# Kernel optimization log

Hardware: AMD Instinct MI355X
Metric: run time of the kernel (lower is better)

## Reference

```python
import jax, jax.numpy as jnp
import numpy as np


def _lstm_last(x, w_ih, w_hh, b_ih, b_hh):
    # x: [M, T, D] -> last hidden state [M, H]; PyTorch gate order i,f,g,o
    M = x.shape[0]
    H = w_hh.shape[1]
    xi = jnp.einsum('mtd,gd->tmg', x, w_ih) + b_ih + b_hh  # [T, M, 4H]
    def step(carry, xt):
        h, c = carry
        gates = xt + h @ w_hh.T
        i, f, g, o = jnp.split(gates, 4, axis=-1)
        c = jax.nn.sigmoid(f) * c + jax.nn.sigmoid(i) * jnp.tanh(g)
        h = jax.nn.sigmoid(o) * jnp.tanh(c)
        return (h, c), None
    z = jnp.zeros((M, H), x.dtype)
    (h, _), _ = jax.lax.scan(step, (z, z), xi)
    return h


def _gcn_conv(x, edge_index, w, b):
    # Symmetric-normalized GCN conv with self loops (PyG GCNConv defaults).
    # x: [BT, N, F] -> [BT, N, Hg]
    N = x.shape[1]
    loops = jnp.arange(N, dtype=edge_index.dtype)
    src = jnp.concatenate([edge_index[0], loops])
    dst = jnp.concatenate([edge_index[1], loops])
    deg = jnp.zeros((N,), x.dtype).at[dst].add(jnp.ones((), x.dtype))
    dinv = jax.lax.rsqrt(deg)  # deg >= 1 thanks to self loops
    norm = (dinv[src] * dinv[dst])[:, None]  # [E+N, 1]
    xw = x @ w                               # [BT, N, Hg]
    msg = xw[:, src, :] * norm               # gather along node axis
    out = jnp.zeros_like(xw).at[:, dst, :].add(msg)  # scatter-add
    return out + b


def setup_inputs() -> dict:
    key = jax.random.key(0)
    ks = jax.random.split(key, 16)
    B, T, N, F = 2, 12, 10000, 16
    Hg, H, P, E = 32, 64, 4, 160000
    sc = 0.1
    return {
        'era5_seq': jax.random.normal(ks[0], (B, T, N, F), jnp.float32),
        'zeta_seq': jax.random.normal(ks[1], (B, T, N), jnp.float32),
        'edge_index': jax.random.randint(ks[2], (2, E), 0, N, jnp.int32),
        'gcn_w': jax.random.normal(ks[3], (F, Hg), jnp.float32) * sc,
        'gcn_b': jnp.zeros((Hg,), jnp.float32),
        'w_ih1': jax.random.normal(ks[4], (4 * H, Hg), jnp.float32) * sc,
        'w_hh1': jax.random.normal(ks[5], (4 * H, H), jnp.float32) * sc,
        'b_ih1': jax.random.normal(ks[6], (4 * H,), jnp.float32) * sc,
        'b_hh1': jax.random.normal(ks[7], (4 * H,), jnp.float32) * sc,
        'w_ih2': jax.random.normal(ks[8], (4 * H, 1), jnp.float32) * sc,
        'w_hh2': jax.random.normal(ks[9], (4 * H, H), jnp.float32) * sc,
        'b_ih2': jax.random.normal(ks[10], (4 * H,), jnp.float32) * sc,
        'b_hh2': jax.random.normal(ks[11], (4 * H,), jnp.float32) * sc,
        'fc_w': jax.random.normal(ks[12], (P, 2 * H), jnp.float32) * sc,
        'fc_b': jnp.zeros((P,), jnp.float32),
    }


def reference(era5_seq, zeta_seq, edge_index, gcn_w, gcn_b, w_ih1, w_hh1, b_ih1, b_hh1, w_ih2, w_hh2, b_ih2, b_hh2, fc_w, fc_b):
    B, T, N, F = era5_seq.shape
    Hg = gcn_w.shape[1]
    # GCN over all (b, t) slices at once (replaces nested python loops)
    h = _gcn_conv(era5_seq.reshape(B * T, N, F), edge_index, gcn_w, gcn_b)
    gcn_seq = h.reshape(B, T, N, Hg).transpose(0, 2, 1, 3).reshape(B * N, T, Hg)
    spatial_feat = _lstm_last(gcn_seq, w_ih1, w_hh1, b_ih1, b_hh1)  # [B*N, H]
    z_seq = zeta_seq.transpose(0, 2, 1).reshape(B * N, T, 1)
    zeta_feat = _lstm_last(z_seq, w_ih2, w_hh2, b_ih2, b_hh2)        # [B*N, H]
    combined = jnp.concatenate([spatial_feat, zeta_feat], axis=-1)
    y = combined @ fc_w.T + fc_b                                     # [B*N, P]
    return y.reshape(B, N, -1).transpose(0, 2, 1)                    # [B, P, N]
```

## Files before the change

kernel.cpp:

```cpp
#include <hip/hip_runtime.h>
#include <hip/hip_bf16.h>
#include <stdint.h>

#define NN 10000
#define EE 160000
#define BB 2
#define TT 12
#define FF 16
#define HG 32
#define HH 64
#define PP 4
#define BT (BB*TT)
#define MM (BB*NN)
#define CAP 96
#define L2E 1.4426950408889634f

typedef _Float16 half8 __attribute__((ext_vector_type(8)));
typedef _Float16 h2 __attribute__((ext_vector_type(2)));
typedef float f32x4 __attribute__((ext_vector_type(4)));

union UP { uint32_t u; h2 h; };

__device__ __forceinline__ float sigm2(float a) {
  return __builtin_amdgcn_rcpf(1.0f + __builtin_amdgcn_exp2f(-a));
}
__device__ __forceinline__ float tanh2(float a) {
  return fmaf(-2.0f, __builtin_amdgcn_rcpf(1.0f + __builtin_amdgcn_exp2f(a)), 1.0f);
}

__global__ void k_fill(const int* __restrict__ eidx, int* __restrict__ cnt,
                       int* __restrict__ csr) {
  int e = blockIdx.x * 256 + threadIdx.x;
  if (e < EE) {
    int d = eidx[EE + e];
    int pos = atomicAdd(&cnt[d], 1);
    if (pos < CAP) csr[d * CAP + pos] = eidx[e];
  }
}

__global__ __launch_bounds__(256) void k_prep(const float* __restrict__ era5,
                                              uint32_t* __restrict__ xt) {
  int D = blockIdx.x * 256 + threadIdx.x;
  int f2 = D & 7;
  int bt = (D >> 3) % BT;
  int n = D / (8 * BT);
  const float* src = era5 + ((size_t)bt * NN + n) * FF + f2 * 2;
  UP u; u.h[0] = (_Float16)src[0]; u.h[1] = (_Float16)src[1];
  xt[D] = u.u;
}

__global__ __launch_bounds__(256) void k_gather(const uint32_t* __restrict__ xt,
                                                const int* __restrict__ csr,
                                                const int* __restrict__ cnt,
                                                const float* __restrict__ gw,
                                                const float* __restrict__ gb,
                                                uint32_t* __restrict__ gout) {
  __shared__ float wsm[FF * HG];
  __shared__ float gbs[HG];
  __shared__ float agg[4][BT][FF];
  const int tid = threadIdx.x;
  wsm[tid] = gw[tid];
  wsm[tid + 256] = gw[tid + 256];
  if (tid < HG) gbs[tid] = gb[tid];

  const int dloc = tid >> 6, lane = tid & 63;
  const int dst = blockIdx.x * 4 + dloc;
  const int cdst = min(cnt[dst], CAP);
  const float dinv_d = rsqrtf((float)cdst + 1.0f);

  float acc[6];
#pragma unroll
  for (int i = 0; i < 6; ++i) acc[i] = 0.f;

  for (int base = 0; base < cdst; base += 64) {
    int mine = base + lane;
    int sv = 0; float dvv = 0.f;
    if (mine < cdst) {
      sv = csr[dst * CAP + mine];
      dvv = rsqrtf((float)cnt[sv] + 1.0f);
    }
    int lim = min(64, cdst - base);
    for (int j = 0; j < lim; ++j) {
      int sj = __shfl(sv, j);
      float dj = __shfl(dvv, j);
      const uint32_t* row = xt + (size_t)sj * 192;
#pragma unroll
      for (int k = 0; k < 3; ++k) {
        UP u; u.u = row[lane + 64 * k];
        acc[2 * k] += (float)u.h[0] * dj;
        acc[2 * k + 1] += (float)u.h[1] * dj;
      }
    }
  }
  const uint32_t* srow = xt + (size_t)dst * 192;
#pragma unroll
  for (int k = 0; k < 3; ++k) {
    UP u; u.u = srow[lane + 64 * k];
    int d0 = lane + 64 * k;
    int bt = d0 >> 3, f = (d0 & 7) * 2;
    agg[dloc][bt][f]     = (acc[2 * k]     + (float)u.h[0] * dinv_d) * dinv_d;
    agg[dloc][bt][f + 1] = (acc[2 * k + 1] + (float)u.h[1] * dinv_d) * dinv_d;
  }
  __syncthreads();
#pragma unroll
  for (int k = 0; k < 3; ++k) {
    int d0 = lane + 64 * k;
    int t = d0 >> 4, c0 = (d0 & 15) * 2;
#pragma unroll
    for (int b = 0; b < 2; ++b) {
      const float* av = agg[dloc][b * TT + t];
      float v0 = gbs[c0], v1 = gbs[c0 + 1];
#pragma unroll
      for (int f = 0; f < FF; ++f) {
        v0 = fmaf(av[f], wsm[f * HG + c0], v0);
        v1 = fmaf(av[f], wsm[f * HG + c0 + 1], v1);
      }
      UP u; u.h[0] = (_Float16)v0; u.h[1] = (_Float16)v1;
      gout[((size_t)(b * NN + dst)) * 192 + d0] = u.u;
    }
  }
}

__global__ __launch_bounds__(256) void k_lstmfc(
    const _Float16* __restrict__ gout, const float* __restrict__ zeta,
    const float* __restrict__ w_ih1, const float* __restrict__ w_hh1,
    const float* __restrict__ b_ih1, const float* __restrict__ b_hh1,
    const float* __restrict__ w_ih2, const float* __restrict__ w_hh2,
    const float* __restrict__ b_ih2, const float* __restrict__ b_hh2,
    const float* __restrict__ fc_w, const float* __restrict__ fc_b,
    float* __restrict__ out) {
  const int m0 = blockIdx.x * 16;
  const int b = (m0 >= NN) ? 1 : 0;
  const int n0 = m0 - b * NN;
  const int tid = threadIdx.x;
  const int wave = tid >> 6;
  const int lane = tid & 63;
  const int col = lane & 15;
  const int quad = lane >> 4;

  half8 Bx[4];
  half8 Bh1[4][2];
  half8 Bh2[4][2];
  float bias1[4], bias2[4], wx[4];
#pragma unroll
  for (int g = 0; g < 4; ++g) {
    const float sc = (g == 2) ? 2.0f * L2E : L2E;
    int ncol = 16 * (wave + 4 * g) + col;
    bias1[g] = (b_ih1[ncol] + b_hh1[ncol]) * sc;
    bias2[g] = (b_ih2[ncol] + b_hh2[ncol]) * sc;
    wx[g] = w_ih2[ncol] * sc;
#pragma unroll
    for (int j = 0; j < 8; ++j)
      Bx[g][j] = (_Float16)(w_ih1[ncol * HG + quad * 8 + j] * sc);
#pragma unroll
    for (int c2 = 0; c2 < 2; ++c2) {
#pragma unroll
      for (int j = 0; j < 8; ++j) {
        Bh1[g][c2][j] = (_Float16)(w_hh1[ncol * HH + c2 * 32 + quad * 8 + j] * sc);
        Bh2[g][c2][j] = (_Float16)(w_hh2[ncol * HH + c2 * 32 + quad * 8 + j] * sc);
      }
    }
  }

  __shared__ float zbuf[TT][16];
  if (tid < TT * 16) {
    int t = tid >> 4, s = tid & 15;
    zbuf[t][s] = zeta[((size_t)b * TT + t) * NN + n0 + s];
  }
  __shared__ __align__(16) _Float16 hb1[2][16 * 72];
  __shared__ __align__(16) _Float16 hb2[2][16 * 72];
  __shared__ float fcb[16][132];

  const _Float16* gbase = gout + (size_t)(m0 + col) * (TT * HG) + quad * 8;
  half8 A0 = *(const half8*)(gbase);

  float c1[4] = {0.f, 0.f, 0.f, 0.f}, c2v[4] = {0.f, 0.f, 0.f, 0.f};
  float h1f[4], h2f[4];

  __syncthreads();

#pragma unroll
  for (int t = 0; t < TT; ++t) {
    const int p = t & 1;
    if (t > 0) {
#pragma unroll
      for (int r = 0; r < 4; ++r) {
        int a = (quad * 4 + r) * 72 + 16 * wave + col;
        hb1[p][a] = (_Float16)h1f[r];
        hb2[p][a] = (_Float16)h2f[r];
      }
    }
    f32x4 a1[4], a2[4];
#pragma unroll
    for (int g = 0; g < 4; ++g) {
      f32x4 ai; ai[0] = bias1[g]; ai[1] = bias1[g]; ai[2] = bias1[g]; ai[3] = bias1[g];
      a1[g] = __builtin_amdgcn_mfma_f32_16x16x32_f16(A0, Bx[g], ai, 0, 0, 0);
#pragma unroll
      for (int r = 0; r < 4; ++r)
        a2[g][r] = fmaf(wx[g], zbuf[t][quad * 4 + r], bias2[g]);
    }
    if (t < TT - 1) A0 = *(const half8*)(gbase + (t + 1) * HG);
    if (t > 0) {
      __syncthreads();
      const half8 A11 = *(const half8*)(&hb1[p][col * 72 + quad * 8]);
      const half8 A21 = *(const half8*)(&hb1[p][col * 72 + 32 + quad * 8]);
      const half8 A12 = *(const half8*)(&hb2[p][col * 72 + quad * 8]);
      const half8 A22 = *(const half8*)(&hb2[p][col * 72 + 32 + quad * 8]);
#pragma unroll
      for (int g = 0; g < 4; ++g) {
        a1[g] = __builtin_amdgcn_mfma_f32_16x16x32_f16(A11, Bh1[g][0], a1[g], 0, 0, 0);
        a1[g] = __builtin_amdgcn_mfma_f32_16x16x32_f16(A21, Bh1[g][1], a1[g], 0, 0, 0);
        a2[g] = __builtin_amdgcn_mfma_f32_16x16x32_f16(A12, Bh2[g][0], a2[g], 0, 0, 0);
        a2[g] = __builtin_amdgcn_mfma_f32_16x16x32_f16(A22, Bh2[g][1], a2[g], 0, 0, 0);
      }
    }
#pragma unroll
    for (int r = 0; r < 4; ++r) {
      float i1 = sigm2(a1[0][r]), f1 = sigm2(a1[1][r]);
      float g1 = tanh2(a1[2][r]), o1 = sigm2(a1[3][r]);
      c1[r] = fmaf(f1, c1[r], i1 * g1);
      h1f[r] = o1 * tanh2(c1[r] * (2.0f * L2E));
      float i2 = sigm2(a2[0][r]), f2 = sigm2(a2[1][r]);
      float g2 = tanh2(a2[2][r]), o2 = sigm2(a2[3][r]);
      c2v[r] = fmaf(f2, c2v[r], i2 * g2);
      h2f[r] = o2 * tanh2(c2v[r] * (2.0f * L2E));
    }
  }
#pragma unroll
  for (int r = 0; r < 4; ++r) {
    fcb[quad * 4 + r][16 * wave + col] = h1f[r];
    fcb[quad * 4 + r][64 + 16 * wave + col] = h2f[r];
  }
  __syncthreads();
  if (tid < 64) {
    int pp = tid >> 4, s = tid & 15;
    const f32x4* wr = (const f32x4*)(fc_w + pp * 128);
    const float* hv = fcb[s];
    float acc = fc_b[pp];
#pragma unroll
    for (int k = 0; k < 32; ++k) {
      f32x4 w4 = wr[k];
      acc += w4[0] * hv[4 * k] + w4[1] * hv[4 * k + 1] +
             w4[2] * hv[4 * k + 2] + w4[3] * hv[4 * k + 3];
    }
    out[((size_t)(b * PP + pp)) * NN + n0 + s] = acc;
  }
}

extern "C" void kernel_launch(void* const* d_in, const int* in_sizes, int n_in,
                              void* d_out, int out_size, void* d_ws, size_t ws_size,
                              hipStream_t stream) {
  (void)in_sizes; (void)n_in; (void)out_size; (void)ws_size;
  const float* era5  = (const float*)d_in[0];
  const float* zeta  = (const float*)d_in[1];
  const int*   eidx  = (const int*)d_in[2];
  const float* gcn_w = (const float*)d_in[3];
  const float* gcn_b = (const float*)d_in[4];
  const float* w_ih1 = (const float*)d_in[5];
  const float* w_hh1 = (const float*)d_in[6];
  const float* b_ih1 = (const float*)d_in[7];
  const float* b_hh1 = (const float*)d_in[8];
  const float* w_ih2 = (const float*)d_in[9];
  const float* w_hh2 = (const float*)d_in[10];
  const float* b_ih2 = (const float*)d_in[11];
  const float* b_hh2 = (const float*)d_in[12];
  const float* fc_w  = (const float*)d_in[13];
  const float* fc_b  = (const float*)d_in[14];
  float* out = (float*)d_out;

  char* ws = (char*)d_ws;
  int*      cnt  = (int*)(ws);
  int*      csr  = (int*)(ws + (64 << 10));
  uint32_t* xt   = (uint32_t*)(ws + (4ull << 20));
  _Float16* gout = (_Float16*)(ws + (12ull << 20));

  hipMemsetAsync(cnt, 0, NN * sizeof(int), stream);
  k_fill<<<EE / 256, 256, 0, stream>>>(eidx, cnt, csr);
  k_prep<<<(NN * BT * 8) / 256, 256, 0, stream>>>(era5, xt);
  k_gather<<<NN / 4, 256, 0, stream>>>(xt, csr, cnt, gcn_w, gcn_b, (uint32_t*)gout);
  k_lstmfc<<<MM / 16, 256, 0, stream>>>(gout, zeta, w_ih1, w_hh1, b_ih1, b_hh1,
                                        w_ih2, w_hh2, b_ih2, b_hh2, fc_w, fc_b, out);
}
```

Measured before the change: 191.0 us.

## Fuse GCN gather and projection into the LSTM kernel via shared memory

Merges the GCN gather/normalize/projection kernel into the LSTM+FC kernel. Each block now aggregates its 16 destination nodes for a single batch, projects them through the GCN weight into shared memory, and feeds the LSTM MFMAs from LDS instead of a global intermediate. This removes one launch and the round trip of the gout buffer through global memory. In exchange, each node's neighbor gather is split across two blocks (one per batch) with half-width rows, the index and degree loads are repeated per batch, and LDS use per block grows, which may lower occupancy.

Measured after the change: 334.5 us. 75.1% more time.

```diff
diff --git a/kernel.cpp b/kernel.cpp
--- a/kernel.cpp
+++ b/kernel.cpp
@@ -49,80 +49,10 @@
   xt[D] = u.u;
 }
 
-__global__ __launch_bounds__(256) void k_gather(const uint32_t* __restrict__ xt,
-                                                const int* __restrict__ csr,
-                                                const int* __restrict__ cnt,
-                                                const float* __restrict__ gw,
-                                                const float* __restrict__ gb,
-                                                uint32_t* __restrict__ gout) {
-  __shared__ float wsm[FF * HG];
-  __shared__ float gbs[HG];
-  __shared__ float agg[4][BT][FF];
-  const int tid = threadIdx.x;
-  wsm[tid] = gw[tid];
-  wsm[tid + 256] = gw[tid + 256];
-  if (tid < HG) gbs[tid] = gb[tid];
-
-  const int dloc = tid >> 6, lane = tid & 63;
-  const int dst = blockIdx.x * 4 + dloc;
-  const int cdst = min(cnt[dst], CAP);
-  const float dinv_d = rsqrtf((float)cdst + 1.0f);
-
-  float acc[6];
-#pragma unroll
-  for (int i = 0; i < 6; ++i) acc[i] = 0.f;
-
-  for (int base = 0; base < cdst; base += 64) {
-    int mine = base + lane;
-    int sv = 0; float dvv = 0.f;
-    if (mine < cdst) {
-      sv = csr[dst * CAP + mine];
-      dvv = rsqrtf((float)cnt[sv] + 1.0f);
-    }
-    int lim = min(64, cdst - base);
-    for (int j = 0; j < lim; ++j) {
-      int sj = __shfl(sv, j);
-      float dj = __shfl(dvv, j);
-      const uint32_t* row = xt + (size_t)sj * 192;
-#pragma unroll
-      for (int k = 0; k < 3; ++k) {
-        UP u; u.u = row[lane + 64 * k];
-        acc[2 * k] += (float)u.h[0] * dj;
-        acc[2 * k + 1] += (float)u.h[1] * dj;
-      }
-    }
-  }
-  const uint32_t* srow = xt + (size_t)dst * 192;
-#pragma unroll
-  for (int k = 0; k < 3; ++k) {
-    UP u; u.u = srow[lane + 64 * k];
-    int d0 = lane + 64 * k;
-    int bt = d0 >> 3, f = (d0 & 7) * 2;
-    agg[dloc][bt][f]     = (acc[2 * k]     + (float)u.h[0] * dinv_d) * dinv_d;
-    agg[dloc][bt][f + 1] = (acc[2 * k + 1] + (float)u.h[1] * dinv_d) * dinv_d;
-  }
-  __syncthreads();
-#pragma unroll
-  for (int k = 0; k < 3; ++k) {
-    int d0 = lane + 64 * k;
-    int t = d0 >> 4, c0 = (d0 & 15) * 2;
-#pragma unroll
-    for (int b = 0; b < 2; ++b) {
-      const float* av = agg[dloc][b * TT + t];
-      float v0 = gbs[c0], v1 = gbs[c0 + 1];
-#pragma unroll
-      for (int f = 0; f < FF; ++f) {
-        v0 = fmaf(av[f], wsm[f * HG + c0], v0);
-        v1 = fmaf(av[f], wsm[f * HG + c0 + 1], v1);
-      }
-      UP u; u.h[0] = (_Float16)v0; u.h[1] = (_Float16)v1;
-      gout[((size_t)(b * NN + dst)) * 192 + d0] = u.u;
-    }
-  }
-}
-
-__global__ __launch_bounds__(256) void k_lstmfc(
-    const _Float16* __restrict__ gout, const float* __restrict__ zeta,
+__global__ __launch_bounds__(256) void k_fused(
+    const uint32_t* __restrict__ xt, const int* __restrict__ csr,
+    const int* __restrict__ cnt, const float* __restrict__ gw,
+    const float* __restrict__ gb, const float* __restrict__ zeta,
     const float* __restrict__ w_ih1, const float* __restrict__ w_hh1,
     const float* __restrict__ b_ih1, const float* __restrict__ b_hh1,
     const float* __restrict__ w_ih2, const float* __restrict__ w_hh2,
@@ -138,6 +68,23 @@
   const int col = lane & 15;
   const int quad = lane >> 4;
 
+  __shared__ float wsm[FF * HG];
+  __shared__ float gbs[HG];
+  __shared__ uint32_t aggd[16 * 96];
+  __shared__ __align__(16) _Float16 xwbuf[16 * 384];
+  __shared__ float zbuf[TT][16];
+  __shared__ __align__(16) _Float16 hb1[2][16 * 72];
+  __shared__ __align__(16) _Float16 hb2[2][16 * 72];
+  __shared__ float fcb[16][132];
+
+  wsm[tid] = gw[tid];
+  wsm[tid + 256] = gw[tid + 256];
+  if (tid < HG) gbs[tid] = gb[tid];
+  if (tid < TT * 16) {
+    int t = tid >> 4, s = tid & 15;
+    zbuf[t][s] = zeta[((size_t)b * TT + t) * NN + n0 + s];
+  }
+
   half8 Bx[4];
   half8 Bh1[4][2];
   half8 Bh2[4][2];
@@ -162,22 +109,77 @@
     }
   }
 
-  __shared__ float zbuf[TT][16];
-  if (tid < TT * 16) {
-    int t = tid >> 4, s = tid & 15;
-    zbuf[t][s] = zeta[((size_t)b * TT + t) * NN + n0 + s];
-  }
-  __shared__ __align__(16) _Float16 hb1[2][16 * 72];
-  __shared__ __align__(16) _Float16 hb2[2][16 * 72];
-  __shared__ float fcb[16][132];
-
-  const _Float16* gbase = gout + (size_t)(m0 + col) * (TT * HG) + quad * 8;
-  half8 A0 = *(const half8*)(gbase);
+  for (int dd = 0; dd < 4; ++dd) {
+    const int sloc = wave * 4 + dd;
+    const int dst = n0 + sloc;
+    const int cdst = min(cnt[dst], CAP);
+    const float dinv_d = rsqrtf((float)cdst + 1.0f);
+    float a0 = 0.f, a1 = 0.f, a2 = 0.f, a3 = 0.f;
+    for (int base = 0; base < cdst; base += 64) {
+      int mine = base + lane;
+      int sv = 0; float dvv = 0.f;
+      if (mine < cdst) {
+        sv = csr[dst * CAP + mine];
+        dvv = rsqrtf((float)cnt[sv] + 1.0f);
+      }
+      int lim = min(64, cdst - base);
+      for (int j = 0; j < lim; ++j) {
+        int sj = __shfl(sv, j);
+        float dj = __shfl(dvv, j);
+        const uint32_t* row = xt + (size_t)sj * 192 + b * 96;
+        UP u0; u0.u = row[lane];
+        a0 = fmaf((float)u0.h[0], dj, a0);
+        a1 = fmaf((float)u0.h[1], dj, a1);
+        if (lane < 32) {
+          UP u1; u1.u = row[64 + lane];
+          a2 = fmaf((float)u1.h[0], dj, a2);
+          a3 = fmaf((float)u1.h[1], dj, a3);
+        }
+      }
+    }
+    const uint32_t* srow = xt + (size_t)dst * 192 + b * 96;
+    UP s0; s0.u = srow[lane];
+    UP w0;
+    w0.h[0] = (_Float16)((a0 + (float)s0.h[0] * dinv_d) * dinv_d);
+    w0.h[1] = (_Float16)((a1 + (float)s0.h[1] * dinv_d) * dinv_d);
+    aggd[sloc * 96 + lane] = w0.u;
+    if (lane < 32) {
+      UP s1; s1.u = srow[64 + lane];
+      UP w1;
+      w1.h[0] = (_Float16)((a2 + (float)s1.h[0] * dinv_d) * dinv_d);
+      w1.h[1] = (_Float16)((a3 + (float)s1.h[1] * dinv_d) * dinv_d);
+      aggd[sloc * 96 + 64 + lane] = w1.u;
+    }
+  }
+  __syncthreads();
+
+  {
+    const int s = tid >> 4, cp = tid & 15;
+#pragma unroll
+    for (int t = 0; t < TT; ++t) {
+      const half8 r0 = *(const half8*)&aggd[s * 96 + t * 8];
+      const half8 r1 = *(const half8*)&aggd[s * 96 + t * 8 + 4];
+      float v0 = gbs[2 * cp], v1 = gbs[2 * cp + 1];
+#pragma unroll
+      for (int f = 0; f < 8; ++f) {
+        float av = (float)r0[f];
+        v0 = fmaf(av, wsm[f * HG + 2 * cp], v0);
+        v1 = fmaf(av, wsm[f * HG + 2 * cp + 1], v1);
+      }
+#pragma unroll
+      for (int f = 0; f < 8; ++f) {
+        float av = (float)r1[f];
+        v0 = fmaf(av, wsm[(8 + f) * HG + 2 * cp], v0);
+        v1 = fmaf(av, wsm[(8 + f) * HG + 2 * cp + 1], v1);
+      }
+      UP u; u.h[0] = (_Float16)v0; u.h[1] = (_Float16)v1;
+      *(uint32_t*)&xwbuf[s * 384 + t * 32 + 2 * cp] = u.u;
+    }
+  }
+  __syncthreads();
 
   float c1[4] = {0.f, 0.f, 0.f, 0.f}, c2v[4] = {0.f, 0.f, 0.f, 0.f};
   float h1f[4], h2f[4];
-
-  __syncthreads();
 
 #pragma unroll
   for (int t = 0; t < TT; ++t) {
@@ -190,6 +192,7 @@
         hb2[p][a] = (_Float16)h2f[r];
       }
     }
+    const half8 A0 = *(const half8*)&xwbuf[col * 384 + t * 32 + quad * 8];
     f32x4 a1[4], a2[4];
 #pragma unroll
     for (int g = 0; g < 4; ++g) {
@@ -199,7 +202,6 @@
       for (int r = 0; r < 4; ++r)
         a2[g][r] = fmaf(wx[g], zbuf[t][quad * 4 + r], bias2[g]);
     }
-    if (t < TT - 1) A0 = *(const half8*)(gbase + (t + 1) * HG);
     if (t > 0) {
       __syncthreads();
       const half8 A11 = *(const half8*)(&hb1[p][col * 72 + quad * 8]);
@@ -269,15 +271,15 @@
   float* out = (float*)d_out;
 
   char* ws = (char*)d_ws;
-  int*      cnt  = (int*)(ws);
-  int*      csr  = (int*)(ws + (64 << 10));
-  uint32_t* xt   = (uint32_t*)(ws + (4ull << 20));
-  _Float16* gout = (_Float16*)(ws + (12ull << 20));
+  int*      cnt = (int*)(ws);
+  int*      csr = (int*)(ws + (64 << 10));
+  uint32_t* xt  = (uint32_t*)(ws + (4ull << 20));
 
   hipMemsetAsync(cnt, 0, NN * sizeof(int), stream);
   k_fill<<<EE / 256, 256, 0, stream>>>(eidx, cnt, csr);
   k_prep<<<(NN * BT * 8) / 256, 256, 0, stream>>>(era5, xt);
-  k_gather<<<NN / 4, 256, 0, stream>>>(xt, csr, cnt, gcn_w, gcn_b, (uint32_t*)gout);
-  k_lstmfc<<<MM / 16, 256, 0, stream>>>(gout, zeta, w_ih1, w_hh1, b_ih1, b_hh1,
-                                        w_ih2, w_hh2, b_ih2, b_hh2, fc_w, fc_b, out);
-}
+  k_fused<<<MM / 16, 256, 0, stream>>>(xt, csr, cnt, gcn_w, gcn_b, zeta,
+                                       w_ih1, w_hh1, b_ih1, b_hh1,
+                                       w_ih2, w_hh2, b_ih2, b_hh2,
+                                       fc_w, fc_b, out);
+}
```
